# Performance work log

Measured on AMD Instinct MI355X. Metric: run time of the kernel, lower is better.

The kernel has to match this reference:

```python
import jax, jax.numpy as jnp
import numpy as np

N, F_IN, HID, E = 100000, 128, 64, 3200000


def setup_inputs() -> dict:
    key = jax.random.key(0)
    ks = jax.random.split(key, 12)
    s = 0.05
    inp = {
        "x": jax.random.normal(ks[0], (N, F_IN), jnp.float32),
        "edge_index": jax.random.randint(ks[1], (2, E), 0, N, dtype=jnp.int32),
        "edge_weight": jax.random.uniform(ks[2], (E,), jnp.float32),
    }
    C = F_IN + HID  # DConv input channels = cat([X, H])
    # DConv weights have shape (2, K, in_channels, out_channels); K = 1 here.
    inp["Wz"] = s * jax.random.normal(ks[3], (2, 1, C, HID), jnp.float32)
    inp["bz"] = jnp.zeros((HID,), jnp.float32)
    inp["Wr"] = s * jax.random.normal(ks[4], (2, 1, C, HID), jnp.float32)
    inp["br"] = jnp.zeros((HID,), jnp.float32)
    inp["Wh"] = s * jax.random.normal(ks[5], (2, 1, C, HID), jnp.float32)
    inp["bh"] = jnp.zeros((HID,), jnp.float32)
    inp["Wlin"] = s * jax.random.normal(ks[6], (HID, 1), jnp.float32)
    inp["blin"] = jnp.zeros((1,), jnp.float32)
    return inp


def _dconv_k1(Y, W, b):
    # DConv with K=1: only the 0-th Chebyshev term of both diffusion
    # directions is used -> Y @ (W[0,0] + W[1,0]) + b. No propagation.
    return jnp.matmul(Y, W[0, 0] + W[1, 0]) + b


def reference(x, edge_index, edge_weight, Wz, bz, Wr, br, Wh, bh, Wlin, blin):
    n = x.shape[0]
    # Faithful-but-unused: original DConv normalizes edge weights by
    # out/in degree before the K>1 check; with K=1 it never affects output.
    row, col = edge_index[0], edge_index[1]
    deg_out = jax.ops.segment_sum(edge_weight, row, num_segments=n)
    deg_in = jax.ops.segment_sum(edge_weight, col, num_segments=n)
    _norm_out = jnp.where(deg_out[row] > 0, edge_weight / deg_out[row], 0.0)
    _norm_in = jnp.where(deg_in[col] > 0, edge_weight / deg_in[col], 0.0)

    H0 = jnp.zeros((n, Wz.shape[-1]), x.dtype)  # _set_hidden_state -> zeros
    XH = jnp.concatenate([x, H0], axis=1)       # [N, F_IN + HID]
    Z = jax.nn.sigmoid(_dconv_k1(XH, Wz, bz))   # update gate
    R = jax.nn.sigmoid(_dconv_k1(XH, Wr, br))   # reset gate
    XRH = jnp.concatenate([x, R * H0], axis=1)
    H_tilde = jnp.tanh(_dconv_k1(XRH, Wh, bh))
    H = Z * H0 + (1.0 - Z) * H_tilde            # GRU state update

    h = jax.nn.relu(H)
    # dropout: identity in eval mode (deterministic reference)
    return jnp.matmul(h, Wlin) + blin            # [N, 1]
```

## Files before the change

kernel.cpp:

```cpp
#include <hip/hip_runtime.h>
#include <hip/hip_bf16.h>

using bf16x8 = __attribute__((ext_vector_type(8))) short;
using f32x4  = __attribute__((ext_vector_type(4))) float;

static constexpr int kN          = 100000;
static constexpr int kFIN        = 128;
static constexpr int kTermStride = 192 * 64;
static constexpr int kTiles      = kN / 16;
static constexpr int kBlocks     = 1024;
static constexpr int kWaves      = kBlocks * 4;

__device__ __forceinline__ short f2bf(float v) {
    union { float f; unsigned u; } a; a.f = v;
    unsigned r = a.u + 0x7fffu + ((a.u >> 16) & 1u);
    return (short)(r >> 16);
}

__device__ __forceinline__ float rcp_fast(float x) { return __builtin_amdgcn_rcpf(x); }
__device__ __forceinline__ float sigmoid_fast(float x) {
    return rcp_fast(1.0f + __expf(-x));
}
__device__ __forceinline__ float tanh_fast(float x) {
    float e = __expf(2.0f * x);
    return 1.0f - 2.0f * rcp_fast(e + 1.0f);
}

__global__ __launch_bounds__(256, 4) void fused_gcn(
    const float* __restrict__ x,
    const float* __restrict__ Wz,
    const float* __restrict__ bz,
    const float* __restrict__ Wh,
    const float* __restrict__ bh,
    const float* __restrict__ wlin,
    const float* __restrict__ blin,
    float* __restrict__ out)
{
    __shared__ short lw[16384];

    const int t    = threadIdx.x;
    const int wid  = t >> 6;
    const int lane = t & 63;
    const int r    = lane & 15;
    const int g    = lane >> 4;
    const int gw   = blockIdx.x * 4 + wid;
    const int t0   = gw;
    const int t1   = (gw + kWaves < kTiles) ? gw + kWaves : -1;

    f32x4 f[8];
    auto load_x = [&](int tile) {
        const float* xrow = x + (size_t)(tile * 16 + r) * kFIN;
        #pragma unroll
        for (int kk = 0; kk < 4; ++kk) {
            f[kk * 2]     = *(const f32x4*)(xrow + kk * 32 + g * 8);
            f[kk * 2 + 1] = *(const f32x4*)(xrow + kk * 32 + g * 8 + 4);
        }
    };

    load_x(t0);

    float bzc[4], bhc[4], wlc[4];
    #pragma unroll
    for (int jt = 0; jt < 4; ++jt) {
        int c = jt * 16 + r;
        bzc[jt] = bz[c]; bhc[jt] = bh[c]; wlc[jt] = wlin[c];
    }
    const float bl = blin[0];

    {
        const int s  = t >> 4;
        const int c0 = (t << 2) & 63;
        char* dstb = (char*)lw +
            ((c0 >> 4) * 512 + (s >> 3) * 128 + (c0 & 15) * 8 + (s & 7)) * 2;
        #pragma unroll
        for (int mat = 0; mat < 2; ++mat) {
            const float* W = mat ? Wh : Wz;
            #pragma unroll
            for (int it = 0; it < 8; ++it) {
                const int fidx = it * 1024 + t * 4;
                f32x4 w0 = *(const f32x4*)(W + fidx);
                f32x4 w1 = *(const f32x4*)(W + kTermStride + fidx);
                const int off = (mat * 8192 + (it >> 1) * 2048 + (it & 1) * 256) * 2;
                #pragma unroll
                for (int i = 0; i < 4; ++i)
                    *(short*)(dstb + off + i * 16) = f2bf(w0[i] + w1[i]);
            }
        }
    }
    __syncthreads();

    bf16x8 a[4];
    auto cvt = [&]() {
        #pragma unroll
        for (int kk = 0; kk < 4; ++kk) {
            #pragma unroll
            for (int e = 0; e < 4; ++e) {
                a[kk][e]     = f2bf(f[kk * 2][e]);
                a[kk][e + 4] = f2bf(f[kk * 2 + 1][e]);
            }
        }
    };

    auto compute_tile = [&](int tile) {
        f32x4 accz[4], acch[4];
        #pragma unroll
        for (int jt = 0; jt < 4; ++jt) {
            accz[jt] = f32x4{0.f, 0.f, 0.f, 0.f};
            acch[jt] = f32x4{0.f, 0.f, 0.f, 0.f};
        }
        #pragma unroll
        for (int kk = 0; kk < 4; ++kk) {
            #pragma unroll
            for (int jt = 0; jt < 4; ++jt) {
                bf16x8 wz = *(const bf16x8*)&lw[(kk * 4 + jt) * 512 + lane * 8];
                bf16x8 wh = *(const bf16x8*)&lw[8192 + (kk * 4 + jt) * 512 + lane * 8];
                accz[jt] = __builtin_amdgcn_mfma_f32_16x16x32_bf16(a[kk], wz, accz[jt], 0, 0, 0);
                acch[jt] = __builtin_amdgcn_mfma_f32_16x16x32_bf16(a[kk], wh, acch[jt], 0, 0, 0);
            }
        }
        float contrib[4] = {0.f, 0.f, 0.f, 0.f};
        #pragma unroll
        for (int jt = 0; jt < 4; ++jt) {
            #pragma unroll
            for (int i = 0; i < 4; ++i) {
                float z  = sigmoid_fast(accz[jt][i] + bzc[jt]);
                float ht = tanh_fast(acch[jt][i] + bhc[jt]);
                float H  = (1.0f - z) * ht;
                contrib[i] += fmaxf(H, 0.f) * wlc[jt];
            }
        }
        #pragma unroll
        for (int m = 1; m < 16; m <<= 1) {
            #pragma unroll
            for (int i = 0; i < 4; ++i)
                contrib[i] += __shfl_xor(contrib[i], m, 64);
        }
        if (r == 0) {
            f32x4 o;
            #pragma unroll
            for (int i = 0; i < 4; ++i) o[i] = contrib[i] + bl;
            *(f32x4*)(out + tile * 16 + g * 4) = o;
        }
    };

    cvt();
    if (t1 >= 0) load_x(t1);
    compute_tile(t0);
    if (t1 >= 0) {
        cvt();
        compute_tile(t1);
    }
}

extern "C" void kernel_launch(void* const* d_in, const int* in_sizes, int n_in,
                              void* d_out, int out_size, void* d_ws, size_t ws_size,
                              hipStream_t stream) {
    const float* x    = (const float*)d_in[0];
    const float* Wz   = (const float*)d_in[3];
    const float* bz   = (const float*)d_in[4];
    const float* Wh   = (const float*)d_in[7];
    const float* bh   = (const float*)d_in[8];
    const float* wlin = (const float*)d_in[9];
    const float* blin = (const float*)d_in[10];

    fused_gcn<<<dim3(kBlocks), dim3(256), 0, stream>>>(
        x, Wz, bz, Wh, bh, wlin, blin, (float*)d_out);
}
```

Measured before the change: 21.07 us.

## Process two tiles per wave with shared LDS weight loads and swizzled layout

Reduces the grid to 768 blocks and gives each wave two adjacent row tiles computed together, so each LDS weight fragment is reused across two MFMAs. Any leftover tiles go to a tail pass. It also XOR-swizzles the LDS weight layout to avoid bank conflicts, converts to bf16 with packed hardware instructions, and replaces the shuffle reduction with DPP row shifts. In exchange it uses more registers (occupancy hint lowered to 3) and loads both tiles up front rather than overlapping the second load with compute.

```diff
diff --git a/kernel.cpp b/kernel.cpp
--- a/kernel.cpp
+++ b/kernel.cpp
@@ -8,8 +8,10 @@
 static constexpr int kFIN        = 128;
 static constexpr int kTermStride = 192 * 64;
 static constexpr int kTiles      = kN / 16;
-static constexpr int kBlocks     = 1024;
+static constexpr int kBlocks     = 768;
 static constexpr int kWaves      = kBlocks * 4;
+static constexpr int kBaseTiles  = kWaves * 2;
+static constexpr int kExtra      = kTiles - kBaseTiles;
 
 __device__ __forceinline__ short f2bf(float v) {
     union { float f; unsigned u; } a; a.f = v;
@@ -17,6 +19,12 @@
     return (short)(r >> 16);
 }
 
+__device__ __forceinline__ unsigned cvt_pk_bf16(float a, float b) {
+    unsigned r;
+    asm("v_cvt_pk_bf16_f32 %0, %1, %2" : "=v"(r) : "v"(a), "v"(b));
+    return r;
+}
+
 __device__ __forceinline__ float rcp_fast(float x) { return __builtin_amdgcn_rcpf(x); }
 __device__ __forceinline__ float sigmoid_fast(float x) {
     return rcp_fast(1.0f + __expf(-x));
@@ -26,7 +34,20 @@
     return 1.0f - 2.0f * rcp_fast(e + 1.0f);
 }
 
-__global__ __launch_bounds__(256, 4) void fused_gcn(
+__device__ __forceinline__ float row16_sum(float v) {
+    int x;
+    x = __builtin_amdgcn_update_dpp(0, __float_as_int(v), 0x128, 0xF, 0xF, false);
+    v += __int_as_float(x);
+    x = __builtin_amdgcn_update_dpp(0, __float_as_int(v), 0x124, 0xF, 0xF, false);
+    v += __int_as_float(x);
+    x = __builtin_amdgcn_update_dpp(0, __float_as_int(v), 0x122, 0xF, 0xF, false);
+    v += __int_as_float(x);
+    x = __builtin_amdgcn_update_dpp(0, __float_as_int(v), 0x121, 0xF, 0xF, false);
+    v += __int_as_float(x);
+    return v;
+}
+
+__global__ __launch_bounds__(256, 3) void fused_gcn(
     const float* __restrict__ x,
     const float* __restrict__ Wz,
     const float* __restrict__ bz,
@@ -44,11 +65,10 @@
     const int r    = lane & 15;
     const int g    = lane >> 4;
     const int gw   = blockIdx.x * 4 + wid;
-    const int t0   = gw;
-    const int t1   = (gw + kWaves < kTiles) ? gw + kWaves : -1;
-
-    f32x4 f[8];
-    auto load_x = [&](int tile) {
+    const int t0   = gw * 2, t1 = t0 + 1;
+    const int t2   = (gw < kExtra) ? kBaseTiles + gw : -1;
+
+    auto load_x = [&](f32x4* f, int tile) {
         const float* xrow = x + (size_t)(tile * 16 + r) * kFIN;
         #pragma unroll
         for (int kk = 0; kk < 4; ++kk) {
@@ -57,7 +77,9 @@
         }
     };
 
-    load_x(t0);
+    f32x4 f0[8], f1[8];
+    load_x(f0, t0);
+    load_x(f1, t1);
 
     float bzc[4], bhc[4], wlc[4];
     #pragma unroll
@@ -68,10 +90,15 @@
     const float bl = blin[0];
 
     {
-        const int s  = t >> 4;
-        const int c0 = (t << 2) & 63;
-        char* dstb = (char*)lw +
-            ((c0 >> 4) * 512 + (s >> 3) * 128 + (c0 & 15) * 8 + (s & 7)) * 2;
+        const int s4  = t >> 4;
+        const int e0  = s4 & 7;
+        const int b7  = (s4 >> 3) & 1;
+        const int jtp = (t & 15) >> 2;
+        const int clb = (t & 3) * 32;
+        const int base_rt = jtp * 512 + b7 * 128 + clb + e0;
+        int rb[4];
+        #pragma unroll
+        for (int i = 0; i < 4; ++i) rb[i] = base_rt + (((i ^ jtp) & 3) << 3);
         #pragma unroll
         for (int mat = 0; mat < 2; ++mat) {
             const float* W = mat ? Wh : Wz;
@@ -80,44 +107,29 @@
                 const int fidx = it * 1024 + t * 4;
                 f32x4 w0 = *(const f32x4*)(W + fidx);
                 f32x4 w1 = *(const f32x4*)(W + kTermStride + fidx);
-                const int off = (mat * 8192 + (it >> 1) * 2048 + (it & 1) * 256) * 2;
+                const int kkb5   = ((it >> 1) & 1) << 5;
+                const int basect = mat * 8192 + (it >> 1) * 2048 + (it & 1) * 256;
                 #pragma unroll
                 for (int i = 0; i < 4; ++i)
-                    *(short*)(dstb + off + i * 16) = f2bf(w0[i] + w1[i]);
+                    lw[(rb[i] ^ kkb5) + basect] = f2bf(w0[i] + w1[i]);
             }
         }
     }
     __syncthreads();
 
-    bf16x8 a[4];
-    auto cvt = [&]() {
+    auto cvt = [&](const f32x4* f, bf16x8* a) {
         #pragma unroll
         for (int kk = 0; kk < 4; ++kk) {
-            #pragma unroll
-            for (int e = 0; e < 4; ++e) {
-                a[kk][e]     = f2bf(f[kk * 2][e]);
-                a[kk][e + 4] = f2bf(f[kk * 2 + 1][e]);
-            }
+            union { unsigned u[4]; bf16x8 v; } p;
+            p.u[0] = cvt_pk_bf16(f[kk * 2][0], f[kk * 2][1]);
+            p.u[1] = cvt_pk_bf16(f[kk * 2][2], f[kk * 2][3]);
+            p.u[2] = cvt_pk_bf16(f[kk * 2 + 1][0], f[kk * 2 + 1][1]);
+            p.u[3] = cvt_pk_bf16(f[kk * 2 + 1][2], f[kk * 2 + 1][3]);
+            a[kk] = p.v;
         }
     };
 
-    auto compute_tile = [&](int tile) {
-        f32x4 accz[4], acch[4];
-        #pragma unroll
-        for (int jt = 0; jt < 4; ++jt) {
-            accz[jt] = f32x4{0.f, 0.f, 0.f, 0.f};
-            acch[jt] = f32x4{0.f, 0.f, 0.f, 0.f};
-        }
-        #pragma unroll
-        for (int kk = 0; kk < 4; ++kk) {
-            #pragma unroll
-            for (int jt = 0; jt < 4; ++jt) {
-                bf16x8 wz = *(const bf16x8*)&lw[(kk * 4 + jt) * 512 + lane * 8];
-                bf16x8 wh = *(const bf16x8*)&lw[8192 + (kk * 4 + jt) * 512 + lane * 8];
-                accz[jt] = __builtin_amdgcn_mfma_f32_16x16x32_bf16(a[kk], wz, accz[jt], 0, 0, 0);
-                acch[jt] = __builtin_amdgcn_mfma_f32_16x16x32_bf16(a[kk], wh, acch[jt], 0, 0, 0);
-            }
-        }
+    auto epilogue = [&](const f32x4* accz, const f32x4* acch, int tile) {
         float contrib[4] = {0.f, 0.f, 0.f, 0.f};
         #pragma unroll
         for (int jt = 0; jt < 4; ++jt) {
@@ -130,11 +142,7 @@
             }
         }
         #pragma unroll
-        for (int m = 1; m < 16; m <<= 1) {
-            #pragma unroll
-            for (int i = 0; i < 4; ++i)
-                contrib[i] += __shfl_xor(contrib[i], m, 64);
-        }
+        for (int i = 0; i < 4; ++i) contrib[i] = row16_sum(contrib[i]);
         if (r == 0) {
             f32x4 o;
             #pragma unroll
@@ -143,12 +151,57 @@
         }
     };
 
-    cvt();
-    if (t1 >= 0) load_x(t1);
-    compute_tile(t0);
-    if (t1 >= 0) {
-        cvt();
-        compute_tile(t1);
+    bf16x8 a0[4], a1[4];
+    cvt(f0, a0);
+    cvt(f1, a1);
+
+    f32x4 accz0[4], acch0[4], accz1[4], acch1[4];
+    #pragma unroll
+    for (int jt = 0; jt < 4; ++jt) {
+        accz0[jt] = f32x4{0.f, 0.f, 0.f, 0.f};
+        acch0[jt] = f32x4{0.f, 0.f, 0.f, 0.f};
+        accz1[jt] = f32x4{0.f, 0.f, 0.f, 0.f};
+        acch1[jt] = f32x4{0.f, 0.f, 0.f, 0.f};
+    }
+    #pragma unroll
+    for (int kk = 0; kk < 4; ++kk) {
+        #pragma unroll
+        for (int jt = 0; jt < 4; ++jt) {
+            const int xs  = ((kk & 1) << 2) | jt;
+            const int off = ((kk * 4 + jt) << 9) + ((lane ^ xs) << 3);
+            bf16x8 wz = *(const bf16x8*)&lw[off];
+            bf16x8 wh = *(const bf16x8*)&lw[8192 + off];
+            accz0[jt] = __builtin_amdgcn_mfma_f32_16x16x32_bf16(a0[kk], wz, accz0[jt], 0, 0, 0);
+            accz1[jt] = __builtin_amdgcn_mfma_f32_16x16x32_bf16(a1[kk], wz, accz1[jt], 0, 0, 0);
+            acch0[jt] = __builtin_amdgcn_mfma_f32_16x16x32_bf16(a0[kk], wh, acch0[jt], 0, 0, 0);
+            acch1[jt] = __builtin_amdgcn_mfma_f32_16x16x32_bf16(a1[kk], wh, acch1[jt], 0, 0, 0);
+        }
+    }
+    epilogue(accz0, acch0, t0);
+    epilogue(accz1, acch1, t1);
+
+    if (t2 >= 0) {
+        load_x(f0, t2);
+        cvt(f0, a0);
+        f32x4 accz[4], acch[4];
+        #pragma unroll
+        for (int jt = 0; jt < 4; ++jt) {
+            accz[jt] = f32x4{0.f, 0.f, 0.f, 0.f};
+            acch[jt] = f32x4{0.f, 0.f, 0.f, 0.f};
+        }
+        #pragma unroll
+        for (int kk = 0; kk < 4; ++kk) {
+            #pragma unroll
+            for (int jt = 0; jt < 4; ++jt) {
+                const int xs  = ((kk & 1) << 2) | jt;
+                const int off = ((kk * 4 + jt) << 9) + ((lane ^ xs) << 3);
+                bf16x8 wz = *(const bf16x8*)&lw[off];
+                bf16x8 wh = *(const bf16x8*)&lw[8192 + off];
+                accz[jt] = __builtin_amdgcn_mfma_f32_16x16x32_bf16(a0[kk], wz, accz[jt], 0, 0, 0);
+                acch[jt] = __builtin_amdgcn_mfma_f32_16x16x32_bf16(a0[kk], wh, acch[jt], 0, 0, 0);
+            }
+        }
+        epilogue(accz, acch, t2);
     }
 }
 
```

Measured after the change: 22.46 us. 1.07x slower.
